# Kernel tuning notes

Hardware: AMD Instinct MI355X
Metric: run time of the kernel (lower is better)

The kernel has to match this reference:

```python
import jax, jax.numpy as jnp
import numpy as np

VOCAB = 4000
U = 30000   # unique tokens
M = 12      # max mid-char length
H = 256     # hidden_size
O = 768     # output_size
B = 16      # sequences
L = 2048    # tokens per sequence (equal lengths -> jit-friendly reassemble)


def setup_inputs() -> dict:
    key = jax.random.key(0)
    ks = jax.random.split(key, 8)
    emb_table = jax.random.normal(ks[0], (VOCAB, H), dtype=jnp.float32)
    emb_table = emb_table.at[0].set(0.0)  # padding_idx=0
    head_w = jax.random.normal(ks[1], (3 * H, O), dtype=jnp.float32) * 0.02
    head_b = jax.random.normal(ks[2], (O,), dtype=jnp.float32) * 0.02
    first = jax.random.randint(ks[3], (U,), 0, VOCAB, dtype=jnp.int32)
    mid = jax.random.randint(ks[4], (U, M), 0, VOCAB, dtype=jnp.int32)
    last = jax.random.randint(ks[5], (U,), 0, VOCAB, dtype=jnp.int32)
    inv_i = jax.random.randint(ks[6], (B * L,), 0, U, dtype=jnp.int32)
    return {"emb_table": emb_table, "head_w": head_w, "head_b": head_b,
            "first": first, "mid": mid, "last": last, "inv_i": inv_i,
            "batch": B, "seq_len": L}


def reference(emb_table, head_w, head_b, first, mid, last, inv_i, batch, seq_len):
    def lookup(ids):
        # emulate padding_idx=0: id 0 contributes a zero vector
        v = emb_table[ids]
        return v * (ids != 0)[..., None].astype(v.dtype)

    rep = jnp.concatenate(
        [lookup(first), lookup(mid).sum(axis=1), lookup(last)], axis=-1)  # [U, 3H]
    out = rep @ head_w + head_b                                           # [U, O]
    tok = out[inv_i].reshape(batch, seq_len, -1)                          # [B, L, O]
    # reassemble: one zero row before and after each sequence (F.pad (1,1) on time)
    return jnp.pad(tok, ((0, 0), (1, 1), (0, 0)))                         # [B, L+2, O]
```

## Files before the change

kernel.cpp:

```cpp
#include <hip/hip_runtime.h>

#define VOCAB 4000
#define UNIQ 30000
#define MIDN 12
#define HID 256
#define OUT 768
#define BATCH 16
#define SEQ 2048

#define NXCD 8
#define XCOLS 96
#define SUBC 16
#define TCHUNK 2048
#define NCHUNK 16
#define TPASS 256
#define NPASS 8
#define PLANE 32008

typedef __attribute__((ext_vector_type(8))) short short8;
typedef __attribute__((ext_vector_type(4))) float f32x4;
typedef __attribute__((ext_vector_type(4))) unsigned int u32x4;
typedef __attribute__((ext_vector_type(4))) unsigned short u16x4;

__device__ __forceinline__ float bitsf(unsigned int x) {
    float f; __builtin_memcpy(&f, &x, 4); return f;
}
__device__ __forceinline__ unsigned short f2bf(float f) {
    unsigned int x;
    __builtin_memcpy(&x, &f, 4);
    x += 0x7fff + ((x >> 16) & 1);
    return (unsigned short)(x >> 16);
}

__global__ __launch_bounds__(256) void prep(
    const float* __restrict__ W, unsigned short* __restrict__ Wt,
    const int* __restrict__ first, const int* __restrict__ mid,
    const int* __restrict__ last, const int* __restrict__ inv_i,
    short* __restrict__ idsT)
{
    __shared__ float T[32][33];
    if (blockIdx.z < 3) {
        const int s  = blockIdx.z;
        const int n0 = blockIdx.x * 32;
        const int h0 = blockIdx.y * 32;
        const int tx = threadIdx.x & 31;
        const int ty = threadIdx.x >> 5;
        #pragma unroll
        for (int k = 0; k < 4; ++k) {
            int h = ty + 8 * k;
            T[h][tx] = W[(size_t)(s * HID + h0 + h) * OUT + n0 + tx];
        }
        __syncthreads();
        #pragma unroll
        for (int k = 0; k < 4; ++k) {
            int n = ty + 8 * k;
            Wt[(size_t)(s * OUT + n0 + n) * HID + h0 + tx] = f2bf(T[tx][n]);
        }
    } else {
        int bid2 = blockIdx.y * 24 + blockIdx.x;
        int t = bid2 * 256 + threadIdx.x;
        if (t >= BATCH * SEQ) return;
        int u = inv_i[t];
        int4 m0 = *reinterpret_cast<const int4*>(&mid[u * MIDN]);
        int4 m1 = *reinterpret_cast<const int4*>(&mid[u * MIDN + 4]);
        int4 m2 = *reinterpret_cast<const int4*>(&mid[u * MIDN + 8]);
        short ids[16];
        ids[0]  = (short)first[u];
        ids[1]  = (short)m0.x; ids[2]  = (short)m0.y; ids[3]  = (short)m0.z; ids[4]  = (short)m0.w;
        ids[5]  = (short)m1.x; ids[6]  = (short)m1.y; ids[7]  = (short)m1.z; ids[8]  = (short)m1.w;
        ids[9]  = (short)m2.x; ids[10] = (short)m2.y; ids[11] = (short)m2.z; ids[12] = (short)m2.w;
        ids[13] = (short)last[u];
        ids[14] = 0; ids[15] = 0;
        *reinterpret_cast<short8*>(&idsT[(size_t)t * 16])     = *reinterpret_cast<short8*>(&ids[0]);
        *reinterpret_cast<short8*>(&idsT[(size_t)t * 16 + 8]) = *reinterpret_cast<short8*>(&ids[8]);
    }
}

__global__ __launch_bounds__(256) void proj_mfma(
    const float* __restrict__ E,
    const unsigned short* __restrict__ Wt,
    unsigned short* __restrict__ P,
    unsigned short* __restrict__ Pmid)
{
    const int s     = blockIdx.z;
    const int vbase = blockIdx.x * 128;
    const int cbase = blockIdx.y * 128;
    const unsigned short* Wts = Wt + (size_t)s * OUT * HID;

    __shared__ short As[128][40];
    __shared__ short Bs[128][40];

    const int tid  = threadIdx.x;
    const int lane = tid & 63;
    const int w    = tid >> 6;
    const int wm   = w >> 1;
    const int wn   = w & 1;
    const int lo   = lane & 15;
    const int hi   = lane >> 4;

    f32x4 acc[4][4] = {};

    for (int kt = 0; kt < HID; kt += 32) {
        #pragma unroll
        for (int p = 0; p < 2; ++p) {
            int idx = p * 256 + tid;
            int row = idx >> 2;
            int ko  = (idx & 3) * 8;
            short8 v = *reinterpret_cast<const short8*>(
                &Wts[(size_t)(cbase + row) * HID + kt + ko]);
            *reinterpret_cast<short8*>(&As[row][ko]) = v;
        }
        #pragma unroll
        for (int p = 0; p < 2; ++p) {
            int idx = p * 256 + tid;
            int row = idx >> 2;
            int ko  = (idx & 3) * 8;
            int gv  = vbase + row;
            f32x4 e0 = {}, e1 = {};
            if (gv < VOCAB) {
                e0 = *reinterpret_cast<const f32x4*>(&E[(size_t)gv * HID + kt + ko]);
                e1 = *reinterpret_cast<const f32x4*>(&E[(size_t)gv * HID + kt + ko + 4]);
            }
            short8 v;
            v[0] = (short)f2bf(e0.x); v[1] = (short)f2bf(e0.y);
            v[2] = (short)f2bf(e0.z); v[3] = (short)f2bf(e0.w);
            v[4] = (short)f2bf(e1.x); v[5] = (short)f2bf(e1.y);
            v[6] = (short)f2bf(e1.z); v[7] = (short)f2bf(e1.w);
            *reinterpret_cast<short8*>(&Bs[row][ko]) = v;
        }
        __syncthreads();

        short8 a[4], b[4];
        #pragma unroll
        for (int f = 0; f < 4; ++f)
            a[f] = *reinterpret_cast<short8*>(&As[wm * 64 + f * 16 + lo][hi * 8]);
        #pragma unroll
        for (int f = 0; f < 4; ++f)
            b[f] = *reinterpret_cast<short8*>(&Bs[wn * 64 + f * 16 + lo][hi * 8]);
        #pragma unroll
        for (int fm = 0; fm < 4; ++fm)
            #pragma unroll
            for (int fn = 0; fn < 4; ++fn)
                acc[fm][fn] = __builtin_amdgcn_mfma_f32_16x16x32_bf16(
                    a[fm], b[fn], acc[fm][fn], 0, 0, 0);
        __syncthreads();
    }

    #pragma unroll
    for (int fm = 0; fm < 4; ++fm) {
        #pragma unroll
        for (int fn = 0; fn < 4; ++fn) {
            const int c0 = cbase + wm * 64 + fm * 16 + hi * 4;
            const int v  = vbase + wn * 64 + fn * 16 + lo;
            if (v < VOCAB) {
                u16x4 vals;
                vals.x = f2bf(acc[fm][fn][0]);
                vals.y = f2bf(acc[fm][fn][1]);
                vals.z = f2bf(acc[fm][fn][2]);
                vals.w = f2bf(acc[fm][fn][3]);
                if (s == 1) {
                    *reinterpret_cast<u16x4*>(
                        &Pmid[((size_t)(c0 >> 4) * VOCAB + v) * SUBC + (c0 & 15)]) = vals;
                } else {
                    const int so = (s == 0) ? 0 : 1;
                    const unsigned int sl = (unsigned int)c0 / XCOLS;
                    const unsigned int cc = (unsigned int)c0 - sl * XCOLS;
                    *reinterpret_cast<u16x4*>(
                        &P[(((size_t)sl * 2 + so) * VOCAB + v) * XCOLS + cc]) = vals;
                }
            }
        }
    }
}

extern __shared__ char lds_raw[];

__global__ __launch_bounds__(1024) void token_lds(
    const unsigned short* __restrict__ P,
    const unsigned short* __restrict__ Pmid,
    const short* __restrict__ idsT,
    const float* __restrict__ bias,
    float* __restrict__ out)
{
    const int xcd = blockIdx.x & 7;
    const int bi  = blockIdx.x >> 3;

    const int tid = threadIdx.x;
    const int l4  = tid & 3;
    const int grp = tid >> 2;

    char* myplane = lds_raw + l4 * PLANE;
    const unsigned short* Pbase = P + (size_t)xcd * 2 * VOCAB * XCOLS;

    if (bi == 0 && tid < 768) {
        int r  = tid / 24;
        int c4 = tid % 24;
        int b  = r >> 1;
        int row = (r & 1) ? (b * (SEQ + 2) + SEQ + 1) : (b * (SEQ + 2));
        f32x4 z = {};
        *reinterpret_cast<f32x4*>(
            &out[(size_t)row * OUT + xcd * XCOLS + c4 * 4]) = z;
    }

    int cur_sl = -1;

    #pragma unroll 1
    for (int k = 0; k < 3; ++k) {
        const int task = bi * 3 + k;
        const int sl   = task >> 4;
        const int ch   = task & 15;

        if (sl != cur_sl) {
            if (cur_sl >= 0) __syncthreads();
            const int sub = xcd * 6 + sl;
            const unsigned short* src = Pmid + (size_t)sub * VOCAB * SUBC;
            #pragma unroll
            for (int i = 0; i < 16; ++i) {
                int idx = i * 1024 + tid;
                if (idx < VOCAB * 4) {
                    int row = idx >> 2;
                    int q   = idx & 3;
                    uint2 v = *reinterpret_cast<const uint2*>(&src[row * SUBC + q * 4]);
                    *reinterpret_cast<uint2*>(lds_raw + q * PLANE + row * 8) = v;
                }
            }
            __syncthreads();
            cur_sl = sl;
        }

        const int csub = sl * SUBC + l4 * 4;
        const int colc = xcd * XCOLS + csub;
        const unsigned short* P0 = Pbase + csub;
        const unsigned short* P2 = Pbase + (size_t)VOCAB * XCOLS + csub;
        const f32x4 bv = *reinterpret_cast<const f32x4*>(&bias[colc]);

        const int t0 = ch * TCHUNK + grp;

#define LDIDS(lo_, hi_, tt_) { \
        const u32x4* _r = reinterpret_cast<const u32x4*>(&idsT[(size_t)(tt_) * 16]); \
        lo_ = _r[0]; hi_ = _r[1]; }

#define GATHER(fv_, lv_, lo_, hi_) { \
        int _fid = (int)((lo_).x & 0xffffu); \
        int _lid = (int)((hi_).z >> 16); \
        fv_ = *reinterpret_cast<const uint2*>(&P0[(size_t)_fid * XCOLS]); \
        lv_ = *reinterpret_cast<const uint2*>(&P2[(size_t)_lid * XCOLS]); }

        u32x4 ilA, ihA, ilB, ihB;
        uint2 fvA, lvA, fvB, lvB;

        LDIDS(ilA, ihA, t0);
        LDIDS(ilB, ihB, t0 + TPASS);
        GATHER(fvA, lvA, ilA, ihA);

        #pragma unroll
        for (int p = 0; p < NPASS; ++p) {
            const bool even = (p & 1) == 0;
            u32x4 clo = even ? ilA : ilB;
            u32x4 chi = even ? ihA : ihB;
            uint2 cfv = even ? fvA : fvB;
            uint2 clv = even ? lvA : lvB;

            if (p + 1 < NPASS) {
                if (even) { GATHER(fvB, lvB, ilB, ihB); }
                else      { GATHER(fvA, lvA, ilA, ihA); }
            }
            if (p + 2 < NPASS) {
                if (even) { LDIDS(ilA, ihA, t0 + (p + 2) * TPASS); }
                else      { LDIDS(ilB, ihB, t0 + (p + 2) * TPASS); }
            }

            int rid[MIDN];
            rid[0]  = (int)(clo.x >> 16);
            rid[1]  = (int)(clo.y & 0xffffu);
            rid[2]  = (int)(clo.y >> 16);
            rid[3]  = (int)(clo.z & 0xffffu);
            rid[4]  = (int)(clo.z >> 16);
            rid[5]  = (int)(clo.w & 0xffffu);
            rid[6]  = (int)(clo.w >> 16);
            rid[7]  = (int)(chi.x & 0xffffu);
            rid[8]  = (int)(chi.x >> 16);
            rid[9]  = (int)(chi.y & 0xffffu);
            rid[10] = (int)(chi.y >> 16);
            rid[11] = (int)(chi.z & 0xffffu);

            uint2 mv[MIDN];
            #pragma unroll
            for (int m = 0; m < MIDN; ++m)
                mv[m] = *reinterpret_cast<const uint2*>(myplane + rid[m] * 8);

            float a0 = bv.x, a1 = bv.y, a2 = bv.z, a3 = bv.w;
            #pragma unroll
            for (int m = 0; m < MIDN; ++m) {
                a0 += bitsf(mv[m].x << 16);
                a1 += bitsf(mv[m].x & 0xffff0000u);
                a2 += bitsf(mv[m].y << 16);
                a3 += bitsf(mv[m].y & 0xffff0000u);
            }
            a0 += bitsf(cfv.x << 16); a1 += bitsf(cfv.x & 0xffff0000u);
            a2 += bitsf(cfv.y << 16); a3 += bitsf(cfv.y & 0xffff0000u);
            a0 += bitsf(clv.x << 16); a1 += bitsf(clv.x & 0xffff0000u);
            a2 += bitsf(clv.y << 16); a3 += bitsf(clv.y & 0xffff0000u);

            const int t = t0 + p * TPASS;
            const int b = t >> 11;
            const int l = t & (SEQ - 1);
            float* dst = &out[((size_t)(b * (SEQ + 2) + l + 1)) * OUT + colc];
            f32x4 o = {a0, a1, a2, a3};
            __builtin_nontemporal_store(o, reinterpret_cast<f32x4*>(dst));
        }
#undef LDIDS
#undef GATHER
    }
}

extern "C" void kernel_launch(void* const* d_in, const int* in_sizes, int n_in,
                              void* d_out, int out_size, void* d_ws, size_t ws_size,
                              hipStream_t stream)
{
    const float* emb    = (const float*)d_in[0];
    const float* head_w = (const float*)d_in[1];
    const float* head_b = (const float*)d_in[2];
    const int*   first  = (const int*)d_in[3];
    const int*   mid    = (const int*)d_in[4];
    const int*   last   = (const int*)d_in[5];
    const int*   inv_i  = (const int*)d_in[6];
    float* out = (float*)d_out;

    char* ws = (char*)d_ws;
    unsigned short* P    = (unsigned short*)ws;
    unsigned short* Wt   = (unsigned short*)(ws + 12288000);
    unsigned short* Pmid = (unsigned short*)(ws + 13467648);
    short*          idsT = (short*)(ws + 19611648);

    dim3 gp(24, 8, 4);
    prep<<<gp, 256, 0, stream>>>(head_w, Wt, first, mid, last, inv_i, idsT);

    dim3 g1(32, 6, 3);
    proj_mfma<<<g1, 256, 0, stream>>>(emb, Wt, P, Pmid);

    token_lds<<<256, 1024, 4 * PLANE, stream>>>(P, Pmid, idsT, head_b, out);
}
```

Before: 63.36 us.

## Precompute bf16 embeddings and byte-offset token ids in prep kernel

Embedding rows are now converted to bf16 once in the prep kernel, so proj_mfma loads bf16 directly instead of converting fp32 in every tile pass (the conversion was repeated for each of 18 column/slice blocks). Token ids are stored as precomputed 32-bit byte offsets, which removes the unpacking and multiplies in the token kernel's inner loop, but doubles the id buffer read per token. The accumulation is also written with 2-wide float vectors, likely aiming at packed FP32 adds.

```diff
diff --git a/kernel.cpp b/kernel.cpp
--- a/kernel.cpp
+++ b/kernel.cpp
@@ -18,6 +18,7 @@
 #define PLANE 32008
 
 typedef __attribute__((ext_vector_type(8))) short short8;
+typedef __attribute__((ext_vector_type(2))) float f32x2;
 typedef __attribute__((ext_vector_type(4))) float f32x4;
 typedef __attribute__((ext_vector_type(4))) unsigned int u32x4;
 typedef __attribute__((ext_vector_type(4))) unsigned short u16x4;
@@ -36,7 +37,8 @@
     const float* __restrict__ W, unsigned short* __restrict__ Wt,
     const int* __restrict__ first, const int* __restrict__ mid,
     const int* __restrict__ last, const int* __restrict__ inv_i,
-    short* __restrict__ idsT)
+    unsigned int* __restrict__ idsO,
+    const float* __restrict__ E, unsigned short* __restrict__ Ebf)
 {
     __shared__ float T[32][33];
     if (blockIdx.z < 3) {
@@ -56,7 +58,7 @@
             int n = ty + 8 * k;
             Wt[(size_t)(s * OUT + n0 + n) * HID + h0 + tx] = f2bf(T[tx][n]);
         }
-    } else {
+    } else if (blockIdx.z == 3) {
         int bid2 = blockIdx.y * 24 + blockIdx.x;
         int t = bid2 * 256 + threadIdx.x;
         if (t >= BATCH * SEQ) return;
@@ -64,20 +66,38 @@
         int4 m0 = *reinterpret_cast<const int4*>(&mid[u * MIDN]);
         int4 m1 = *reinterpret_cast<const int4*>(&mid[u * MIDN + 4]);
         int4 m2 = *reinterpret_cast<const int4*>(&mid[u * MIDN + 8]);
-        short ids[16];
-        ids[0]  = (short)first[u];
-        ids[1]  = (short)m0.x; ids[2]  = (short)m0.y; ids[3]  = (short)m0.z; ids[4]  = (short)m0.w;
-        ids[5]  = (short)m1.x; ids[6]  = (short)m1.y; ids[7]  = (short)m1.z; ids[8]  = (short)m1.w;
-        ids[9]  = (short)m2.x; ids[10] = (short)m2.y; ids[11] = (short)m2.z; ids[12] = (short)m2.w;
-        ids[13] = (short)last[u];
-        ids[14] = 0; ids[15] = 0;
-        *reinterpret_cast<short8*>(&idsT[(size_t)t * 16])     = *reinterpret_cast<short8*>(&ids[0]);
-        *reinterpret_cast<short8*>(&idsT[(size_t)t * 16 + 8]) = *reinterpret_cast<short8*>(&ids[8]);
+        unsigned int o[16];
+        o[0]  = (unsigned int)m0.x * 8u;  o[1]  = (unsigned int)m0.y * 8u;
+        o[2]  = (unsigned int)m0.z * 8u;  o[3]  = (unsigned int)m0.w * 8u;
+        o[4]  = (unsigned int)m1.x * 8u;  o[5]  = (unsigned int)m1.y * 8u;
+        o[6]  = (unsigned int)m1.z * 8u;  o[7]  = (unsigned int)m1.w * 8u;
+        o[8]  = (unsigned int)m2.x * 8u;  o[9]  = (unsigned int)m2.y * 8u;
+        o[10] = (unsigned int)m2.z * 8u;  o[11] = (unsigned int)m2.w * 8u;
+        o[12] = (unsigned int)first[u] * (XCOLS * 2u);
+        o[13] = (unsigned int)last[u]  * (XCOLS * 2u);
+        o[14] = 0u; o[15] = 0u;
+        u32x4* dst = reinterpret_cast<u32x4*>(&idsO[(size_t)t * 16]);
+        dst[0] = *reinterpret_cast<u32x4*>(&o[0]);
+        dst[1] = *reinterpret_cast<u32x4*>(&o[4]);
+        dst[2] = *reinterpret_cast<u32x4*>(&o[8]);
+        dst[3] = *reinterpret_cast<u32x4*>(&o[12]);
+    } else {
+        int bid2 = (blockIdx.z - 4) * 192 + blockIdx.y * 24 + blockIdx.x;
+        int i = bid2 * 256 + threadIdx.x;
+        if (i >= VOCAB * HID / 8) return;
+        f32x4 e0 = *reinterpret_cast<const f32x4*>(&E[(size_t)i * 8]);
+        f32x4 e1 = *reinterpret_cast<const f32x4*>(&E[(size_t)i * 8 + 4]);
+        short8 v;
+        v[0] = (short)f2bf(e0.x); v[1] = (short)f2bf(e0.y);
+        v[2] = (short)f2bf(e0.z); v[3] = (short)f2bf(e0.w);
+        v[4] = (short)f2bf(e1.x); v[5] = (short)f2bf(e1.y);
+        v[6] = (short)f2bf(e1.z); v[7] = (short)f2bf(e1.w);
+        *reinterpret_cast<short8*>(&Ebf[(size_t)i * 8]) = v;
     }
 }
 
 __global__ __launch_bounds__(256) void proj_mfma(
-    const float* __restrict__ E,
+    const unsigned short* __restrict__ Ebf,
     const unsigned short* __restrict__ Wt,
     unsigned short* __restrict__ P,
     unsigned short* __restrict__ Pmid)
@@ -116,16 +136,9 @@
             int row = idx >> 2;
             int ko  = (idx & 3) * 8;
             int gv  = vbase + row;
-            f32x4 e0 = {}, e1 = {};
-            if (gv < VOCAB) {
-                e0 = *reinterpret_cast<const f32x4*>(&E[(size_t)gv * HID + kt + ko]);
-                e1 = *reinterpret_cast<const f32x4*>(&E[(size_t)gv * HID + kt + ko + 4]);
-            }
-            short8 v;
-            v[0] = (short)f2bf(e0.x); v[1] = (short)f2bf(e0.y);
-            v[2] = (short)f2bf(e0.z); v[3] = (short)f2bf(e0.w);
-            v[4] = (short)f2bf(e1.x); v[5] = (short)f2bf(e1.y);
-            v[6] = (short)f2bf(e1.z); v[7] = (short)f2bf(e1.w);
+            short8 v = {};
+            if (gv < VOCAB)
+                v = *reinterpret_cast<const short8*>(&Ebf[(size_t)gv * HID + kt + ko]);
             *reinterpret_cast<short8*>(&Bs[row][ko]) = v;
         }
         __syncthreads();
@@ -178,7 +191,7 @@
 __global__ __launch_bounds__(1024) void token_lds(
     const unsigned short* __restrict__ P,
     const unsigned short* __restrict__ Pmid,
-    const short* __restrict__ idsT,
+    const unsigned int* __restrict__ idsO,
     const float* __restrict__ bias,
     float* __restrict__ out)
 {
@@ -230,83 +243,82 @@
 
         const int csub = sl * SUBC + l4 * 4;
         const int colc = xcd * XCOLS + csub;
-        const unsigned short* P0 = Pbase + csub;
-        const unsigned short* P2 = Pbase + (size_t)VOCAB * XCOLS + csub;
+        const char* P0 = reinterpret_cast<const char*>(Pbase + csub);
+        const char* P2 = reinterpret_cast<const char*>(Pbase + (size_t)VOCAB * XCOLS + csub);
         const f32x4 bv = *reinterpret_cast<const f32x4*>(&bias[colc]);
 
         const int t0 = ch * TCHUNK + grp;
 
-#define LDIDS(lo_, hi_, tt_) { \
-        const u32x4* _r = reinterpret_cast<const u32x4*>(&idsT[(size_t)(tt_) * 16]); \
-        lo_ = _r[0]; hi_ = _r[1]; }
-
-#define GATHER(fv_, lv_, lo_, hi_) { \
-        int _fid = (int)((lo_).x & 0xffffu); \
-        int _lid = (int)((hi_).z >> 16); \
-        fv_ = *reinterpret_cast<const uint2*>(&P0[(size_t)_fid * XCOLS]); \
-        lv_ = *reinterpret_cast<const uint2*>(&P2[(size_t)_lid * XCOLS]); }
-
-        u32x4 ilA, ihA, ilB, ihB;
+#define LDIDS(m0_, m1_, m2_, fl_, tt_) { \
+        const u32x4* _r = reinterpret_cast<const u32x4*>(&idsO[(size_t)(tt_) * 16]); \
+        m0_ = _r[0]; m1_ = _r[1]; m2_ = _r[2]; fl_ = _r[3]; }
+
+#define GATHER(fv_, lv_, fl_) { \
+        fv_ = *reinterpret_cast<const uint2*>(P0 + (fl_).x); \
+        lv_ = *reinterpret_cast<const uint2*>(P2 + (fl_).y); }
+
+        u32x4 mA0, mA1, mA2, flA, mB0, mB1, mB2, flB;
         uint2 fvA, lvA, fvB, lvB;
 
-        LDIDS(ilA, ihA, t0);
-        LDIDS(ilB, ihB, t0 + TPASS);
-        GATHER(fvA, lvA, ilA, ihA);
+        LDIDS(mA0, mA1, mA2, flA, t0);
+        LDIDS(mB0, mB1, mB2, flB, t0 + TPASS);
+        GATHER(fvA, lvA, flA);
 
         #pragma unroll
         for (int p = 0; p < NPASS; ++p) {
             const bool even = (p & 1) == 0;
-            u32x4 clo = even ? ilA : ilB;
-            u32x4 chi = even ? ihA : ihB;
+            u32x4 c0 = even ? mA0 : mB0;
+            u32x4 c1 = even ? mA1 : mB1;
+            u32x4 c2 = even ? mA2 : mB2;
             uint2 cfv = even ? fvA : fvB;
             uint2 clv = even ? lvA : lvB;
 
             if (p + 1 < NPASS) {
-                if (even) { GATHER(fvB, lvB, ilB, ihB); }
-                else      { GATHER(fvA, lvA, ilA, ihA); }
+                if (even) { GATHER(fvB, lvB, flB); }
+                else      { GATHER(fvA, lvA, flA); }
             }
             if (p + 2 < NPASS) {
-                if (even) { LDIDS(ilA, ihA, t0 + (p + 2) * TPASS); }
-                else      { LDIDS(ilB, ihB, t0 + (p + 2) * TPASS); }
-            }
-
-            int rid[MIDN];
-            rid[0]  = (int)(clo.x >> 16);
-            rid[1]  = (int)(clo.y & 0xffffu);
-            rid[2]  = (int)(clo.y >> 16);
-            rid[3]  = (int)(clo.z & 0xffffu);
-            rid[4]  = (int)(clo.z >> 16);
-            rid[5]  = (int)(clo.w & 0xffffu);
-            rid[6]  = (int)(clo.w >> 16);
-            rid[7]  = (int)(chi.x & 0xffffu);
-            rid[8]  = (int)(chi.x >> 16);
-            rid[9]  = (int)(chi.y & 0xffffu);
-            rid[10] = (int)(chi.y >> 16);
-            rid[11] = (int)(chi.z & 0xffffu);
+                if (even) { LDIDS(mA0, mA1, mA2, flA, t0 + (p + 2) * TPASS); }
+                else      { LDIDS(mB0, mB1, mB2, flB, t0 + (p + 2) * TPASS); }
+            }
 
             uint2 mv[MIDN];
-            #pragma unroll
-            for (int m = 0; m < MIDN; ++m)
-                mv[m] = *reinterpret_cast<const uint2*>(myplane + rid[m] * 8);
-
-            float a0 = bv.x, a1 = bv.y, a2 = bv.z, a3 = bv.w;
+            mv[0]  = *reinterpret_cast<const uint2*>(myplane + c0.x);
+            mv[1]  = *reinterpret_cast<const uint2*>(myplane + c0.y);
+            mv[2]  = *reinterpret_cast<const uint2*>(myplane + c0.z);
+            mv[3]  = *reinterpret_cast<const uint2*>(myplane + c0.w);
+            mv[4]  = *reinterpret_cast<const uint2*>(myplane + c1.x);
+            mv[5]  = *reinterpret_cast<const uint2*>(myplane + c1.y);
+            mv[6]  = *reinterpret_cast<const uint2*>(myplane + c1.z);
+            mv[7]  = *reinterpret_cast<const uint2*>(myplane + c1.w);
+            mv[8]  = *reinterpret_cast<const uint2*>(myplane + c2.x);
+            mv[9]  = *reinterpret_cast<const uint2*>(myplane + c2.y);
+            mv[10] = *reinterpret_cast<const uint2*>(myplane + c2.z);
+            mv[11] = *reinterpret_cast<const uint2*>(myplane + c2.w);
+
+            f32x2 acc01 = {bv.x, bv.y};
+            f32x2 acc23 = {bv.z, bv.w};
             #pragma unroll
             for (int m = 0; m < MIDN; ++m) {
-                a0 += bitsf(mv[m].x << 16);
-                a1 += bitsf(mv[m].x & 0xffff0000u);
-                a2 += bitsf(mv[m].y << 16);
-                a3 += bitsf(mv[m].y & 0xffff0000u);
-            }
-            a0 += bitsf(cfv.x << 16); a1 += bitsf(cfv.x & 0xffff0000u);
-            a2 += bitsf(cfv.y << 16); a3 += bitsf(cfv.y & 0xffff0000u);
-            a0 += bitsf(clv.x << 16); a1 += bitsf(clv.x & 0xffff0000u);
-            a2 += bitsf(clv.y << 16); a3 += bitsf(clv.y & 0xffff0000u);
+                f32x2 v0 = {bitsf(mv[m].x << 16), bitsf(mv[m].x & 0xffff0000u)};
+                f32x2 v1 = {bitsf(mv[m].y << 16), bitsf(mv[m].y & 0xffff0000u)};
+                acc01 += v0;
+                acc23 += v1;
+            }
+            {
+                f32x2 v0 = {bitsf(cfv.x << 16), bitsf(cfv.x & 0xffff0000u)};
+                f32x2 v1 = {bitsf(cfv.y << 16), bitsf(cfv.y & 0xffff0000u)};
+                acc01 += v0; acc23 += v1;
+                f32x2 w0 = {bitsf(clv.x << 16), bitsf(clv.x & 0xffff0000u)};
+                f32x2 w1 = {bitsf(clv.y << 16), bitsf(clv.y & 0xffff0000u)};
+                acc01 += w0; acc23 += w1;
+            }
 
             const int t = t0 + p * TPASS;
             const int b = t >> 11;
             const int l = t & (SEQ - 1);
             float* dst = &out[((size_t)(b * (SEQ + 2) + l + 1)) * OUT + colc];
-            f32x4 o = {a0, a1, a2, a3};
+            f32x4 o = {acc01.x, acc01.y, acc23.x, acc23.y};
             __builtin_nontemporal_store(o, reinterpret_cast<f32x4*>(dst));
         }
 #undef LDIDS
@@ -330,14 +342,16 @@
     char* ws = (char*)d_ws;
     unsigned short* P    = (unsigned short*)ws;
     unsigned short* Wt   = (unsigned short*)(ws + 12288000);
-    unsigned short* Pmid = (unsigned short*)(ws + 13467648);
-    short*          idsT = (short*)(ws + 19611648);
-
-    dim3 gp(24, 8, 4);
-    prep<<<gp, 256, 0, stream>>>(head_w, Wt, first, mid, last, inv_i, idsT);
+    unsigned short* Ebf  = (unsigned short*)(ws + 13467648);
+    unsigned short* Pmid = (unsigned short*)(ws + 15515648);
+    unsigned int*   idsO = (unsigned int*)(ws + 21659648);
+
+    dim3 gp(24, 8, 7);
+    prep<<<gp, 256, 0, stream>>>(head_w, Wt, first, mid, last, inv_i,
+                                 idsO, emb, Ebf);
 
     dim3 g1(32, 6, 3);
-    proj_mfma<<<g1, 256, 0, stream>>>(emb, Wt, P, Pmid);
-
-    token_lds<<<256, 1024, 4 * PLANE, stream>>>(P, Pmid, idsT, head_b, out);
-}
+    proj_mfma<<<g1, 256, 0, stream>>>(Ebf, Wt, P, Pmid);
+
+    token_lds<<<256, 1024, 4 * PLANE, stream>>>(P, Pmid, idsO, head_b, out);
+}
```

Result: slower. 66.13 us (+4.4%).
